# Kernel optimization log

Measured on AMD Instinct MI355X. Metric: run time of the kernel, lower is better.

Reference implementation:

```python
import jax, jax.numpy as jnp
import numpy as np

# --- ConductanceLIFConfig defaults (normalized units, threshold = 1.0) ---
DT_MS = 1.0
C_M = 1.0
G_L = 0.05
E_L = 0.0
E_E = 3.0
E_I = -0.5
E_ADAPT = -0.5
V_RESET = 0.0
TAU_E = 5.0
TAU_I = 10.0
TAU_ADAPT = 100.0
ADAPT_INC = 0.0
NOISE_STD = 0.02
NOISE_TAU = 5.0

GE_DECAY = float(np.exp(-DT_MS / TAU_E))
GI_DECAY = float(np.exp(-DT_MS / TAU_I))
GA_DECAY = float(np.exp(-DT_MS / TAU_ADAPT))
OU_ALPHA = float(np.exp(-DT_MS / NOISE_TAU))
OU_SIGMA = float(NOISE_STD * np.sqrt(1.0 - OU_ALPHA ** 2))  # stationary-variance OU drive

T = 512
N = 65536


def setup_inputs() -> dict:
    key = jax.random.key(0)
    k1, k2, k3, k4 = jax.random.split(key, 4)
    # synaptic conductance inputs per step, normalized by g_L (sparse-ish, small positive)
    g_exc = 0.2 * jax.random.uniform(k1, (T, N), dtype=jnp.float32)
    g_inh = 0.1 * jax.random.uniform(k2, (T, N), dtype=jnp.float32)
    noise = jax.random.normal(k3, (T, N), dtype=jnp.float32)  # white driver for OU process
    v_threshold = jnp.ones((N,), dtype=jnp.float32)
    # tau_ref ~ Normal(5, 2) clamped to [3.0, 8.0], as in __init__
    tau_ref = jnp.clip(5.0 + 2.0 * jax.random.normal(k4, (N,), dtype=jnp.float32), 3.0, 8.0)
    return {"g_exc": g_exc, "g_inh": g_inh, "noise": noise,
            "v_threshold": v_threshold, "tau_ref": tau_ref}


def reference(g_exc, g_inh, noise, v_threshold, tau_ref):
    """T-step conductance-based LIF scan. Returns (spikes [T,N] bool, membranes [T,N] f32)."""

    def step(carry, inp):
        v, gE, gI, gA, ref, ou = carry
        ge_in, gi_in, z = inp
        # exponential conductance decay + input accumulation (units of g_L)
        gE = gE * GE_DECAY + ge_in
        gI = gI * GI_DECAY + gi_in
        gA = gA * GA_DECAY
        # exponential-Euler membrane update toward V_inf
        g_tot_rel = 1.0 + gE + gI + gA                      # total conductance / g_L
        v_inf = (E_L + gE * E_E + gI * E_I + gA * E_ADAPT) / g_tot_rel
        decay = jnp.exp(-(DT_MS * G_L / C_M) * g_tot_rel)
        v = v_inf + (v - v_inf) * decay
        # OU membrane noise
        ou = ou * OU_ALPHA + OU_SIGMA * z
        v = v + ou
        # refractory clamp
        in_ref = ref > 0.0
        v = jnp.where(in_ref, V_RESET, v)
        # spike, reset, refractory restart, adaptation increment
        spike = (v >= v_threshold) & (~in_ref)
        v = jnp.where(spike, V_RESET, v)
        ref = jnp.where(spike, tau_ref, jnp.maximum(ref - DT_MS, 0.0))
        gA = gA + ADAPT_INC * spike.astype(v.dtype)
        return (v, gE, gI, gA, ref, ou), (spike, v)

    z = jnp.zeros((N,), dtype=jnp.float32)
    carry0 = (z, z, z, z, z, z)  # v, g_E, g_I, g_adapt, refractory, ou
    _, (spikes, membranes) = jax.lax.scan(step, carry0, (g_exc, g_inh, noise))
    return spikes, membranes
```

## Files before the change

kernel.cpp:

```cpp
#include <hip/hip_runtime.h>
#include <cmath>


#ifndef PFD
#define PFD 16
#endif

__global__ __launch_bounds__(256, 1) void lif_scan(
    const float* __restrict__ g_exc,
    const float* __restrict__ g_inh,
    const float* __restrict__ noise,
    const float* __restrict__ v_th,
    const float* __restrict__ tau_ref,
    float* __restrict__ out_spk,
    float* __restrict__ out_mem,
    int N, int T,
    float cGE, float cGI, float cALPHA, float cSIGMA)
{
    const int n = blockIdx.x * blockDim.x + threadIdx.x;
    if (n >= N) return;

    const float vth = v_th[n];
    const float trf = tau_ref[n];

    float v = 0.0f, gE = 0.0f, gI = 0.0f, ref = 0.0f, ou = 0.0f;

    const float* __restrict__ pge = g_exc + n;
    const float* __restrict__ pgi = g_inh + n;
    const float* __restrict__ pz  = noise + n;

    auto step = [&](float ge_in, float gi_in, float z, int tt) {
        gE = __fadd_rn(__fmul_rn(gE, cGE), ge_in);
        gI = __fadd_rn(__fmul_rn(gI, cGI), gi_in);

        const float gt  = __fadd_rn(__fadd_rn(1.0f, gE), gI);
        const float num = __fadd_rn(__fmul_rn(gE, 3.0f), __fmul_rn(gI, -0.5f));
        const float vinf = __fdiv_rn(num, gt);

        const float darg = __fmul_rn(-0.05f, gt);
        const float decay = expf(darg);

        v = __fadd_rn(vinf, __fmul_rn(__fsub_rn(v, vinf), decay));

        ou = __fadd_rn(__fmul_rn(ou, cALPHA), __fmul_rn(cSIGMA, z));
        v = __fadd_rn(v, ou);

        const bool in_ref = (ref > 0.0f);
        if (in_ref) v = 0.0f;

        const bool spike = (v >= vth) && (!in_ref);
        if (spike) v = 0.0f;
        ref = spike ? trf : fmaxf(__fsub_rn(ref, 1.0f), 0.0f);

        const size_t off = (size_t)tt * (size_t)N + (size_t)n;
        __builtin_nontemporal_store(spike ? 1.0f : 0.0f, out_spk + off);
        __builtin_nontemporal_store(v, out_mem + off);
    };

    float Age[PFD], Agi[PFD], Az[PFD];
    float Bge[PFD], Bgi[PFD], Bz[PFD];

    #pragma unroll
    for (int i = 0; i < PFD; ++i) {
        const size_t off = (size_t)i * (size_t)N;
        Age[i] = pge[off]; Agi[i] = pgi[off]; Az[i] = pz[off];
    }

    for (int t = 0; t < T; t += 2 * PFD) {
        #pragma unroll
        for (int i = 0; i < PFD; ++i) {
            int tp = t + PFD + i; tp = tp < T ? tp : T - 1;
            const size_t off = (size_t)tp * (size_t)N;
            Bge[i] = pge[off]; Bgi[i] = pgi[off]; Bz[i] = pz[off];
        }
        __builtin_amdgcn_sched_barrier(0);
        #pragma unroll
        for (int i = 0; i < PFD; ++i)
            step(Age[i], Agi[i], Az[i], t + i);

        #pragma unroll
        for (int i = 0; i < PFD; ++i) {
            int tp = t + 2 * PFD + i; tp = tp < T ? tp : T - 1;
            const size_t off = (size_t)tp * (size_t)N;
            Age[i] = pge[off]; Agi[i] = pgi[off]; Az[i] = pz[off];
        }
        __builtin_amdgcn_sched_barrier(0);
        #pragma unroll
        for (int i = 0; i < PFD; ++i)
            step(Bge[i], Bgi[i], Bz[i], t + PFD + i);
    }
}

extern "C" void kernel_launch(void* const* d_in, const int* in_sizes, int n_in,
                              void* d_out, int out_size, void* d_ws, size_t ws_size,
                              hipStream_t stream) {
    const float* g_exc   = (const float*)d_in[0];
    const float* g_inh   = (const float*)d_in[1];
    const float* noise   = (const float*)d_in[2];
    const float* v_th    = (const float*)d_in[3];
    const float* tau_ref = (const float*)d_in[4];

    const int N = in_sizes[3];
    const int T = in_sizes[0] / N;

    float* out_spk = (float*)d_out;
    float* out_mem = (float*)d_out + (size_t)T * (size_t)N;

    const double ge_decay = exp(-1.0 / 5.0);
    const double gi_decay = exp(-1.0 / 10.0);
    const double ou_alpha = exp(-1.0 / 5.0);
    const double ou_sigma = 0.02 * sqrt(1.0 - ou_alpha * ou_alpha);

    const int block = 256;
    const int grid = (N + block - 1) / block;
    lif_scan<<<grid, block, 0, stream>>>(
        g_exc, g_inh, noise, v_th, tau_ref, out_spk, out_mem,
        N, T,
        (float)ge_decay, (float)gi_decay, (float)ou_alpha, (float)ou_sigma);
}
```

Measured before the change: 129.5 us.

## Process two neurons per thread with float2 vector loads and stores

Each thread now simulates a pair of adjacent neurons and uses 64-bit vector loads for the inputs and 64-bit nontemporal stores for the spike and membrane outputs. This halves the thread count, and the block size and prefetch depth are reduced to match. The aim is fewer, wider memory instructions on a bandwidth-bound scan. The trade-off is fewer resident waves to hide memory latency, and the code assumes N is even.

```diff
diff --git a/kernel.cpp b/kernel.cpp
--- a/kernel.cpp
+++ b/kernel.cpp
@@ -3,10 +3,12 @@
 
 
 #ifndef PFD
-#define PFD 16
+#define PFD 8
 #endif
 
-__global__ __launch_bounds__(256, 1) void lif_scan(
+typedef float f32x2 __attribute__((ext_vector_type(2)));
+
+__global__ __launch_bounds__(128, 1) void lif_scan(
     const float* __restrict__ g_exc,
     const float* __restrict__ g_inh,
     const float* __restrict__ noise,
@@ -17,19 +19,25 @@
     int N, int T,
     float cGE, float cGI, float cALPHA, float cSIGMA)
 {
-    const int n = blockIdx.x * blockDim.x + threadIdx.x;
-    if (n >= N) return;
+    const int tid = blockIdx.x * blockDim.x + threadIdx.x;
+    const int N2 = N >> 1;
+    if (tid >= N2) return;
 
-    const float vth = v_th[n];
-    const float trf = tau_ref[n];
+    const f32x2* __restrict__ pge = reinterpret_cast<const f32x2*>(g_exc) + tid;
+    const f32x2* __restrict__ pgi = reinterpret_cast<const f32x2*>(g_inh) + tid;
+    const f32x2* __restrict__ pz  = reinterpret_cast<const f32x2*>(noise) + tid;
+    f32x2* __restrict__ pspk = reinterpret_cast<f32x2*>(out_spk) + tid;
+    f32x2* __restrict__ pmem = reinterpret_cast<f32x2*>(out_mem) + tid;
 
-    float v = 0.0f, gE = 0.0f, gI = 0.0f, ref = 0.0f, ou = 0.0f;
+    const f32x2 vth2 = reinterpret_cast<const f32x2*>(v_th)[tid];
+    const f32x2 trf2 = reinterpret_cast<const f32x2*>(tau_ref)[tid];
 
-    const float* __restrict__ pge = g_exc + n;
-    const float* __restrict__ pgi = g_inh + n;
-    const float* __restrict__ pz  = noise + n;
+    float v0 = 0.f, gE0 = 0.f, gI0 = 0.f, ref0 = 0.f, ou0 = 0.f;
+    float v1 = 0.f, gE1 = 0.f, gI1 = 0.f, ref1 = 0.f, ou1 = 0.f;
 
-    auto step = [&](float ge_in, float gi_in, float z, int tt) {
+    auto one = [&](float& v, float& gE, float& gI, float& ref, float& ou,
+                   float ge_in, float gi_in, float z,
+                   float vth, float trf) -> float {
         gE = __fadd_rn(__fmul_rn(gE, cGE), ge_in);
         gI = __fadd_rn(__fmul_rn(gI, cGI), gi_in);
 
@@ -51,18 +59,26 @@
         const bool spike = (v >= vth) && (!in_ref);
         if (spike) v = 0.0f;
         ref = spike ? trf : fmaxf(__fsub_rn(ref, 1.0f), 0.0f);
-
-        const size_t off = (size_t)tt * (size_t)N + (size_t)n;
-        __builtin_nontemporal_store(spike ? 1.0f : 0.0f, out_spk + off);
-        __builtin_nontemporal_store(v, out_mem + off);
+        return spike ? 1.0f : 0.0f;
     };
 
-    float Age[PFD], Agi[PFD], Az[PFD];
-    float Bge[PFD], Bgi[PFD], Bz[PFD];
+    auto step = [&](f32x2 ge_in, f32x2 gi_in, f32x2 z, int tt) {
+        f32x2 spk, vm;
+        spk.x = one(v0, gE0, gI0, ref0, ou0, ge_in.x, gi_in.x, z.x, vth2.x, trf2.x);
+        vm.x = v0;
+        spk.y = one(v1, gE1, gI1, ref1, ou1, ge_in.y, gi_in.y, z.y, vth2.y, trf2.y);
+        vm.y = v1;
+        const size_t off = (size_t)tt * (size_t)N2;
+        __builtin_nontemporal_store(spk, pspk + off);
+        __builtin_nontemporal_store(vm,  pmem + off);
+    };
+
+    f32x2 Age[PFD], Agi[PFD], Az[PFD];
+    f32x2 Bge[PFD], Bgi[PFD], Bz[PFD];
 
     #pragma unroll
     for (int i = 0; i < PFD; ++i) {
-        const size_t off = (size_t)i * (size_t)N;
+        const size_t off = (size_t)i * (size_t)N2;
         Age[i] = pge[off]; Agi[i] = pgi[off]; Az[i] = pz[off];
     }
 
@@ -70,7 +86,7 @@
         #pragma unroll
         for (int i = 0; i < PFD; ++i) {
             int tp = t + PFD + i; tp = tp < T ? tp : T - 1;
-            const size_t off = (size_t)tp * (size_t)N;
+            const size_t off = (size_t)tp * (size_t)N2;
             Bge[i] = pge[off]; Bgi[i] = pgi[off]; Bz[i] = pz[off];
         }
         __builtin_amdgcn_sched_barrier(0);
@@ -81,7 +97,7 @@
         #pragma unroll
         for (int i = 0; i < PFD; ++i) {
             int tp = t + 2 * PFD + i; tp = tp < T ? tp : T - 1;
-            const size_t off = (size_t)tp * (size_t)N;
+            const size_t off = (size_t)tp * (size_t)N2;
             Age[i] = pge[off]; Agi[i] = pgi[off]; Az[i] = pz[off];
         }
         __builtin_amdgcn_sched_barrier(0);
@@ -111,8 +127,9 @@
     const double ou_alpha = exp(-1.0 / 5.0);
     const double ou_sigma = 0.02 * sqrt(1.0 - ou_alpha * ou_alpha);
 
-    const int block = 256;
-    const int grid = (N + block - 1) / block;
+    const int block = 128;
+    const int pairs = N / 2;
+    const int grid = (pairs + block - 1) / block;
     lif_scan<<<grid, block, 0, stream>>>(
         g_exc, g_inh, noise, v_th, tau_ref, out_spk, out_mem,
         N, T,
```

Result: slower. 161.8 us (+25.0%).
